# Performance work log

Measured on AMD Instinct MI355X. Metric: run time of the kernel, lower is better.

Reference implementation:

```python
import jax, jax.numpy as jnp
import numpy as np

T, B, F = 512, 256, 1
H = 256          # hidden width of all GRU stacks
P = 256          # pred_classes
DELAY = 1
W_SCALE = 0.06   # ~1/sqrt(H), mimics torch GRUCell init scale


def setup_inputs() -> dict:
    key = jax.random.key(0)
    ks = jax.random.split(key, 24)
    rn = lambda k, shp, s=1.0: s * jax.random.normal(k, shp, dtype=jnp.float32)
    return {
        "sequence": rn(ks[0], (T, B, F)),
        "delay_pad": rn(ks[1], (DELAY, B, F)),
        "h0_enc": rn(ks[2], (B, H)),
        "h0_mask": rn(ks[3], (B, H)),
        "h0_pred": rn(ks[4], (B, H)),
        "enc_w_ih": rn(ks[5], (3 * H, F), W_SCALE),
        "enc_w_hh": rn(ks[6], (3 * H, H), W_SCALE),
        "enc_b_ih": rn(ks[7], (3 * H,), W_SCALE),
        "enc_b_hh": rn(ks[8], (3 * H,), W_SCALE),
        "mdec_w_ih": rn(ks[9], (3 * H, H), W_SCALE),
        "mdec_w_hh": rn(ks[10], (3 * H, H), W_SCALE),
        "mdec_b_ih": rn(ks[11], (3 * H,), W_SCALE),
        "mdec_b_hh": rn(ks[12], (3 * H,), W_SCALE),
        "mlin_w": rn(ks[13], (F, H), W_SCALE),
        "mlin_b": rn(ks[14], (F,), W_SCALE),
        "pdec_w_ih": rn(ks[15], (3 * H, H), W_SCALE),
        "pdec_w_hh": rn(ks[16], (3 * H, H), W_SCALE),
        "pdec_b_ih": rn(ks[17], (3 * H,), W_SCALE),
        "pdec_b_hh": rn(ks[18], (3 * H,), W_SCALE),
        "plin_w": rn(ks[19], (P, H), W_SCALE),
        "plin_b": rn(ks[20], (P,), W_SCALE),
    }


def gru_cell(x, h, w_ih, w_hh, b_ih, b_hh):
    # torch.nn.GRUCell semantics; gate order r, z, n in the stacked weights.
    gi = x @ w_ih.T + b_ih           # [B, 3H]
    gh = h @ w_hh.T + b_hh           # [B, 3H]
    i_r, i_z, i_n = jnp.split(gi, 3, axis=-1)
    h_r, h_z, h_n = jnp.split(gh, 3, axis=-1)
    r = jax.nn.sigmoid(i_r + h_r)
    z = jax.nn.sigmoid(i_z + h_z)
    n = jnp.tanh(i_n + r * h_n)
    return (1.0 - z) * n + z * h


def reference(sequence, delay_pad, h0_enc, h0_mask, h0_pred,
              enc_w_ih, enc_w_hh, enc_b_ih, enc_b_hh,
              mdec_w_ih, mdec_w_hh, mdec_b_ih, mdec_b_hh, mlin_w, mlin_b,
              pdec_w_ih, pdec_w_hh, pdec_b_ih, pdec_b_hh, plin_w, plin_b):
    # delay: prepend padding, drop last `delay` steps.  seq stays [T, B, F].
    seq = jnp.concatenate([delay_pad, sequence[:-DELAY]], axis=0)

    def step(carry, x_t):
        h_e, h_m, h_p = carry
        h_e = gru_cell(x_t, h_e, enc_w_ih, enc_w_hh, enc_b_ih, enc_b_hh)
        h_m = gru_cell(h_e, h_m, mdec_w_ih, mdec_w_hh, mdec_b_ih, mdec_b_hh)
        mask_t = h_m @ mlin_w.T + mlin_b      # [B, F]
        h_p = gru_cell(h_e, h_p, pdec_w_ih, pdec_w_hh, pdec_b_ih, pdec_b_hh)
        pred_t = h_p @ plin_w.T + plin_b      # [B, P]
        return (h_e, h_m, h_p), (mask_t, pred_t)

    _, (masks, preds) = jax.lax.scan(step, (h0_enc, h0_mask, h0_pred), seq)
    mask = masks.reshape(seq.shape)           # [T, B, F]
    pred = jnp.mean(preds, axis=0)            # [B, P]
    return mask, pred
```

## Files before the change

kernel.cpp:

```cpp
#include <hip/hip_runtime.h>
#include <hip/hip_fp16.h>

typedef _Float16 f16;
typedef _Float16 f16x8 __attribute__((ext_vector_type(8)));
typedef _Float16 f16x4 __attribute__((ext_vector_type(4)));
typedef float    f32x4 __attribute__((ext_vector_type(4)));

#define TT 512
#define BB 256
#define HH 256

#define O_WFRAG_ENC 0u
#define O_WFRAG_M   393216u
#define O_WFRAG_P   786432u
#define O_WFRAG_GI  1179648u
#define O_HE_ST     1966080u
#define O_HM_ST     2097152u
#define O_HP_ST     2228224u
#define O_HPSUM     2359296u
#define O_DYN       2621440u
#define DYN_PER_STEP 917504u

__device__ __forceinline__ float sigf(float x){ return 1.0f/(1.0f+__expf(-x)); }
__device__ __forceinline__ float tanh_(float x){
  float xc = fminf(fmaxf(x,-15.f),15.f);
  float e  = __expf(2.f*xc);
  return (e-1.f)/(e+1.f);
}
__device__ __forceinline__ int hswz(int row, int j){
  return row*256 + ((((j>>3) ^ (row&7)))<<3) + (j&7);
}
__device__ __forceinline__ void gload_lds16(const void* g, void* l){
  __builtin_amdgcn_global_load_lds(
      (const __attribute__((address_space(1))) unsigned int*)g,
      (__attribute__((address_space(3))) unsigned int*)l, 16, 0, 0);
}
#define SB()        __builtin_amdgcn_sched_barrier(0)
#define LGKM0_SB()  do{ asm volatile("s_waitcnt lgkmcnt(0)" ::: "memory"); SB(); }while(0)
#define WAITV6_SB() do{ asm volatile("s_waitcnt vmcnt(6)"   ::: "memory"); SB(); }while(0)

__global__ void prep_kernel(
    const float* __restrict__ enc_whh, const float* __restrict__ mdec_whh,
    const float* __restrict__ pdec_whh, const float* __restrict__ mdec_wih,
    const float* __restrict__ pdec_wih,
    const float* __restrict__ h0e, const float* __restrict__ h0m, const float* __restrict__ h0p,
    f16* __restrict__ wfrag_enc, f16* __restrict__ wfrag_m, f16* __restrict__ wfrag_p,
    f16* __restrict__ wfrag_gi,
    f16* __restrict__ he_st, f16* __restrict__ hm_st, f16* __restrict__ hp_st,
    float* __restrict__ hpsum)
{
  int idx = blockIdx.x*256 + threadIdx.x;
  const int NW = 8*48*64*8;
  if (idx < 3*NW){
    int b = idx / NW, e = idx % NW;
    int jj = e & 7, l = (e>>3)&63, c = e>>9;
    int ks = c / 48, rem = c % 48;
    int w = rem / 3, g = rem % 3;
    int row = g*256 + w*16 + (l&15);
    int col = ks*32 + (l>>4)*8 + jj;
    const float* W = (b==0)?enc_whh:((b==1)?mdec_whh:pdec_whh);
    f16* D = (b==0)?wfrag_enc:((b==1)?wfrag_m:wfrag_p);
    D[e] = (f16)W[row*256+col];
    return;
  }
  idx -= 3*NW;
  const int NG = 96*8*64*8;
  if (idx < NG){
    int e = idx;
    int jj = e&7, l=(e>>3)&63, ks=(e>>9)&7, mt = e>>12;
    int row = mt*16 + (l&15);
    int col = ks*32 + (l>>4)*8 + jj;
    float v = (row < 768) ? mdec_wih[row*256+col] : pdec_wih[(row-768)*256+col];
    wfrag_gi[e] = (f16)v;
    return;
  }
  idx -= NG;
  if (idx < 65536){
    he_st[idx] = (f16)h0e[idx];
    hm_st[idx] = (f16)h0m[idx];
    hp_st[idx] = (f16)h0p[idx];
    hpsum[idx] = 0.f;
  }
}

template<int MODE>
__device__ __forceinline__ void gru_run(
  int bt, int slice, int SL,
  const f16* __restrict__ wfrag,
  const float* __restrict__ bih, const float* __restrict__ bhh,
  const float* __restrict__ enc_wih,
  const float* __restrict__ seq, const float* __restrict__ dpad,
  const f16* __restrict__ gi_src,
  f16* __restrict__ h_state,
  f16* __restrict__ he_buf,
  const float* __restrict__ mlin_w, const float* __restrict__ mlin_b,
  float* __restrict__ out_mask,
  float* __restrict__ hpsum,
  unsigned char* smem)
{
  const int tid = threadIdx.x;
  const int lane = tid & 63;
  const int wid  = tid >> 6;
  const int l15  = lane & 15;
  const int lhi  = lane >> 4;
  const int bi0  = lhi*4;
  const int b0   = bt*16;
  const int w0   = wid*2;

  f16* wbuf = (f16*)smem;
  f16* hbuf = (f16*)(smem + 98304);
  float* xb   = (float*)(smem + 98304 + 16384);
  float* mred = xb + 32;

  float cr[2], cz[2], cnh[2], cni[2];
  float wr_[2], wz_[2], wn_[2], mw[2];
  #pragma unroll
  for (int q=0;q<2;++q){
    const int j = (w0+q)*16 + l15;
    if (MODE==0){
      cr[q]  = bih[j]     + bhh[j];
      cz[q]  = bih[256+j] + bhh[256+j];
      cnh[q] = bhh[512+j];
      cni[q] = bih[512+j];
      wr_[q]=enc_wih[j]; wz_[q]=enc_wih[256+j]; wn_[q]=enc_wih[512+j];
    } else {
      cr[q]  = bhh[j];
      cz[q]  = bhh[256+j];
      cnh[q] = bhh[512+j];
      cni[q] = 0.f;
    }
    if (MODE==1){ mw[q]=mlin_w[j]; }
  }
  #pragma unroll
  for (int q=0;q<2;++q){
    const int j = (w0+q)*16 + l15;
    #pragma unroll
    for (int r=0;r<4;++r)
      hbuf[hswz(bi0+r, j)] = h_state[(size_t)(b0+bi0+r)*256 + j];
  }
  if (MODE==0 && tid<16){
    const int t = slice*SL;
    xb[tid] = (t==0) ? dpad[b0+tid] : seq[(size_t)(t-1)*BB + b0 + tid];
  }
  #pragma unroll
  for (int q=0;q<2;++q)
    #pragma unroll
    for (int g=0;g<3;++g){
      const int fo = ((w0+q)*3+g)*1024;
      gload_lds16((const char*)wfrag + fo + (lane<<4), (char*)wbuf + fo);
    }
  __syncthreads();

  float psum[2][4];
  if (MODE==2){
    #pragma unroll
    for (int q=0;q<2;++q)
      #pragma unroll
      for (int r=0;r<4;++r) psum[q][r]=0.f;
  }

  for (int ts=0; ts<SL; ++ts){
    const int cur = ts & 1;
    f16* hc = hbuf + cur*4096;
    f16* hn = hbuf + (cur^1)*4096;

    f16x4 gv[2][3];
    if (MODE!=0){
      const f16* gts = gi_src + (size_t)ts*393216u;
      #pragma unroll
      for (int q=0;q<2;++q)
        #pragma unroll
        for (int g=0;g<3;++g)
          gv[q][g] = *(const f16x4*)(gts + ((size_t)(g*256 + (w0+q)*16 + l15))*16 + bi0);
    } else if (tid<16 && ts+1<SL){
      xb[(cur^1)*16 + tid] = seq[(size_t)(slice*SL + ts)*BB + b0 + tid];
    }
    if (MODE==1 && tid<16 && ts>0){
      float v = mlin_b[0];
      #pragma unroll
      for (int w=0;w<8;++w) v += mred[(cur^1)*128 + w*16 + tid];
      out_mask[(size_t)(slice*SL + ts-1)*BB + b0 + tid] = v;
    }

    f32x4 acc[2][3];
    #pragma unroll
    for (int q=0;q<2;++q){
      acc[q][0] = (f32x4){cr[q],cr[q],cr[q],cr[q]};
      acc[q][1] = (f32x4){cz[q],cz[q],cz[q],cz[q]};
      acc[q][2] = (f32x4){cnh[q],cnh[q],cnh[q],cnh[q]};
    }
    #pragma unroll
    for (int k=0;k<8;++k){
      LGKM0_SB();
      {
        const int nk = (k<7) ? (k+1) : 0;
        const char* src = (const char*)wfrag + (size_t)nk*49152u;
        char* dst = (char*)wbuf + (nk&1)*49152;
        #pragma unroll
        for (int q=0;q<2;++q)
          #pragma unroll
          for (int g=0;g<3;++g){
            const int fo = ((w0+q)*3+g)*1024;
            gload_lds16(src + fo + (lane<<4), dst + fo);
          }
      }
      SB();
      if (k>0) WAITV6_SB();

      const f16* wb = wbuf + (k&1)*24576;
      const f16x8 a = *(const f16x8*)(hc + l15*256 + ((((k*4+lhi) ^ (l15&7)))<<3));
      #pragma unroll
      for (int q=0;q<2;++q)
        #pragma unroll
        for (int g=0;g<3;++g){
          const f16x8 b = *(const f16x8*)(wb + (((w0+q)*3+g)*64 + lane)*8);
          acc[q][g] = __builtin_amdgcn_mfma_f32_16x16x32_f16(a, b, acc[q][g], 0,0,0);
        }
    }

    float mpart[4] = {0.f,0.f,0.f,0.f};
    #pragma unroll
    for (int q=0;q<2;++q){
      const int j = (w0+q)*16 + l15;
      float gir[4], giz[4], gin[4];
      if (MODE==0){
        #pragma unroll
        for (int r=0;r<4;++r){
          const float x = xb[cur*16 + bi0 + r];
          gir[r]=x*wr_[q]; giz[r]=x*wz_[q]; gin[r]=x*wn_[q] + cni[q];
        }
      } else {
        #pragma unroll
        for (int r=0;r<4;++r){
          gir[r]=(float)gv[q][0][r]; giz[r]=(float)gv[q][1][r]; gin[r]=(float)gv[q][2][r];
        }
      }
      #pragma unroll
      for (int r=0;r<4;++r){
        const int sz = hswz(bi0+r, j);
        const float hprev = (float)hc[sz];
        const float rr = sigf(gir[r] + acc[q][0][r]);
        const float zz = sigf(giz[r] + acc[q][1][r]);
        const float nn = tanh_(gin[r] + rr*acc[q][2][r]);
        const float h  = (1.f-zz)*nn + zz*hprev;
        hn[sz] = (f16)h;
        if (MODE==0) he_buf[((size_t)ts*BB + (b0+bi0+r))*HH + j] = (f16)h;
        if (MODE==1) mpart[r] += h*mw[q];
        if (MODE==2) psum[q][r] += h;
      }
    }
    if (MODE==1){
      #pragma unroll
      for (int m=1;m<16;m<<=1){
        #pragma unroll
        for (int r=0;r<4;++r) mpart[r] += __shfl_xor(mpart[r], m, 64);
      }
      if (l15==0){
        #pragma unroll
        for (int r=0;r<4;++r) mred[cur*128 + wid*16 + bi0 + r] = mpart[r];
      }
    }
    __syncthreads();
  }

  if (MODE==1 && tid<16){
    float v = mlin_b[0];
    #pragma unroll
    for (int w=0;w<8;++w) v += mred[((SL-1)&1)*128 + w*16 + tid];
    out_mask[(size_t)(slice*SL + SL-1)*BB + b0 + tid] = v;
  }
  {
    const f16* hf = hbuf + (SL&1)*4096;
    #pragma unroll
    for (int q=0;q<2;++q){
      const int j = (w0+q)*16 + l15;
      #pragma unroll
      for (int r=0;r<4;++r)
        h_state[(size_t)(b0+bi0+r)*256 + j] = hf[hswz(bi0+r, j)];
    }
  }
  if (MODE==2){
    #pragma unroll
    for (int q=0;q<2;++q){
      const int j = (w0+q)*16 + l15;
      #pragma unroll
      for (int r=0;r<4;++r){
        const size_t idx = (size_t)(b0+bi0+r)*256 + j;
        hpsum[idx] = hpsum[idx] + psum[q][r];
      }
    }
  }
}

__global__ __launch_bounds__(512) void rec_kernel(
  const float* __restrict__ seq, const float* __restrict__ dpad,
  const float* __restrict__ enc_wih, const float* __restrict__ enc_bih, const float* __restrict__ enc_bhh,
  const float* __restrict__ mdec_bhh, const float* __restrict__ pdec_bhh,
  const float* __restrict__ mlin_w, const float* __restrict__ mlin_b,
  const f16* __restrict__ wfrag_enc, const f16* __restrict__ wfrag_m, const f16* __restrict__ wfrag_p,
  f16* __restrict__ he_st, f16* __restrict__ hm_st, f16* __restrict__ hp_st,
  f16* __restrict__ he_buf, const f16* __restrict__ gi_buf,
  float* __restrict__ hpsum, float* __restrict__ out_mask,
  int dec_slice, int enc_slice, int SL)
{
  __shared__ __align__(16) unsigned char smem[98304 + 16384 + 128 + 1024 + 256];
  const int pp = blockIdx.x;
  if (pp < 16){
    if (dec_slice < 0) return;
    const int bt = pp;
    gru_run<1>(bt, dec_slice, SL, wfrag_m, nullptr, mdec_bhh, nullptr, nullptr, nullptr,
               gi_buf + (size_t)bt*1536*16, hm_st, nullptr, mlin_w, mlin_b, out_mask, nullptr, smem);
  } else if (pp < 32){
    if (dec_slice < 0) return;
    const int bt = pp - 16;
    gru_run<2>(bt, dec_slice, SL, wfrag_p, nullptr, pdec_bhh, nullptr, nullptr, nullptr,
               gi_buf + ((size_t)bt*1536 + 768)*16, hp_st, nullptr, nullptr, nullptr, nullptr, hpsum, smem);
  } else {
    if (enc_slice < 0) return;
    const int bt = pp - 32;
    gru_run<0>(bt, enc_slice, SL, wfrag_enc, enc_bih, enc_bhh, enc_wih, seq, dpad,
               nullptr, he_st, he_buf, nullptr, nullptr, nullptr, nullptr, smem);
  }
}

__global__ __launch_bounds__(256,4) void gi_kernel(
  const f16* __restrict__ he_buf, const f16* __restrict__ wfrag_gi,
  const float* __restrict__ mdec_bih, const float* __restrict__ pdec_bih,
  f16* __restrict__ gi_buf)
{
  const int ts = blockIdx.x >> 2;
  const int bq = blockIdx.x & 3;
  const int tid = threadIdx.x, lane = tid&63, wid = tid>>6;
  const int l15 = lane&15, lhi = lane>>4;
  __shared__ f16 het[64*264];
  {
    const uint4* src = (const uint4*)(he_buf + ((size_t)ts*BB + bq*64)*HH);
    uint4* dst = (uint4*)het;
    #pragma unroll
    for (int k=0;k<8;++k){
      const int i = tid + k*256;
      dst[(i>>5)*33 + (i&31)] = src[i];
    }
  }
  __syncthreads();
  for (int mi=0; mi<24; ++mi){
    const int mt = wid*24 + mi;
    const int row0 = mt*16 + lhi*4;
    float bb[4];
    #pragma unroll
    for (int r=0;r<4;++r){
      const int rw = row0 + r;
      bb[r] = (rw < 768) ? mdec_bih[rw] : pdec_bih[rw-768];
    }
    f32x4 acc[4] = {{0,0,0,0},{0,0,0,0},{0,0,0,0},{0,0,0,0}};
    #pragma unroll
    for (int ks=0;ks<8;++ks){
      const f16x8 a = *(const f16x8*)(wfrag_gi + ((size_t)(mt*8+ks)*64 + lane)*8);
      #pragma unroll
      for (int bt=0;bt<4;++bt){
        const f16x8 b = *(const f16x8*)(het + (bt*16+l15)*264 + ks*32 + lhi*8);
        acc[bt] = __builtin_amdgcn_mfma_f32_16x16x32_f16(a, b, acc[bt], 0,0,0);
      }
    }
    #pragma unroll
    for (int bt=0;bt<4;++bt){
      const int btg = bq*4 + bt;
      const size_t base = (((size_t)ts*16 + btg)*1536 + (size_t)mt*16 + lhi*4)*16 + l15;
      #pragma unroll
      for (int r=0;r<4;++r) gi_buf[base + (size_t)r*16] = (f16)(acc[bt][r] + bb[r]);
    }
  }
}

__global__ __launch_bounds__(256,1) void pred_kernel(
  const float* __restrict__ hpsum, const float* __restrict__ plin_w,
  const float* __restrict__ plin_b, float* __restrict__ out)
{
  __shared__ float hs[256];
  const int p = threadIdx.x;
  const float bias = plin_b[p];
  for (int bb=0; bb<4; ++bb){
    const int b = blockIdx.x*4 + bb;
    __syncthreads();
    hs[p] = hpsum[(size_t)b*256 + p];
    __syncthreads();
    float acc = 0.f;
    const float4* wrow = (const float4*)(plin_w + (size_t)p*256);
    #pragma unroll 4
    for (int k4=0;k4<64;++k4){
      const float4 w = wrow[k4];
      acc += hs[k4*4+0]*w.x + hs[k4*4+1]*w.y + hs[k4*4+2]*w.z + hs[k4*4+3]*w.w;
    }
    out[131072 + (size_t)b*256 + p] = acc*(1.f/512.f) + bias;
  }
}

extern "C" void kernel_launch(void* const* d_in, const int* in_sizes, int n_in,
                              void* d_out, int out_size, void* d_ws, size_t ws_size,
                              hipStream_t stream)
{
  const float* seq      = (const float*)d_in[0];
  const float* dpad     = (const float*)d_in[1];
  const float* h0e      = (const float*)d_in[2];
  const float* h0m      = (const float*)d_in[3];
  const float* h0p      = (const float*)d_in[4];
  const float* enc_wih  = (const float*)d_in[5];
  const float* enc_whh  = (const float*)d_in[6];
  const float* enc_bih  = (const float*)d_in[7];
  const float* enc_bhh  = (const float*)d_in[8];
  const float* mdec_wih = (const float*)d_in[9];
  const float* mdec_whh = (const float*)d_in[10];
  const float* mdec_bih = (const float*)d_in[11];
  const float* mdec_bhh = (const float*)d_in[12];
  const float* mlin_w   = (const float*)d_in[13];
  const float* mlin_b   = (const float*)d_in[14];
  const float* pdec_wih = (const float*)d_in[15];
  const float* pdec_whh = (const float*)d_in[16];
  const float* pdec_bih = (const float*)d_in[17];
  const float* pdec_bhh = (const float*)d_in[18];
  const float* plin_w   = (const float*)d_in[19];
  const float* plin_b   = (const float*)d_in[20];
  float* out = (float*)d_out;

  char* ws = (char*)d_ws;
  f16* wfrag_enc = (f16*)(ws + O_WFRAG_ENC);
  f16* wfrag_m   = (f16*)(ws + O_WFRAG_M);
  f16* wfrag_p   = (f16*)(ws + O_WFRAG_P);
  f16* wfrag_gi  = (f16*)(ws + O_WFRAG_GI);
  f16* he_st     = (f16*)(ws + O_HE_ST);
  f16* hm_st     = (f16*)(ws + O_HM_ST);
  f16* hp_st     = (f16*)(ws + O_HP_ST);
  float* hpsum   = (float*)(ws + O_HPSUM);

  int SL = 64;
  while (SL > 1 && (size_t)O_DYN + (size_t)SL*DYN_PER_STEP > ws_size) SL >>= 1;
  const int S = TT / SL;
  f16* he_buf = (f16*)(ws + O_DYN);
  f16* gi_buf = (f16*)(ws + O_DYN + (size_t)SL*131072u);

  prep_kernel<<<dim3(4096), dim3(256), 0, stream>>>(
      enc_whh, mdec_whh, pdec_whh, mdec_wih, pdec_wih, h0e, h0m, h0p,
      wfrag_enc, wfrag_m, wfrag_p, wfrag_gi, he_st, hm_st, hp_st, hpsum);

  rec_kernel<<<dim3(48), dim3(512), 0, stream>>>(
      seq, dpad, enc_wih, enc_bih, enc_bhh, mdec_bhh, pdec_bhh,
      mlin_w, mlin_b, wfrag_enc, wfrag_m, wfrag_p, he_st, hm_st, hp_st,
      he_buf, gi_buf, hpsum, out, -1, 0, SL);
  gi_kernel<<<dim3(SL*4), dim3(256), 0, stream>>>(he_buf, wfrag_gi, mdec_bih, pdec_bih, gi_buf);

  for (int s=0; s<S; ++s){
    const int enc_s = (s+1 < S) ? (s+1) : -1;
    rec_kernel<<<dim3(48), dim3(512), 0, stream>>>(
        seq, dpad, enc_wih, enc_bih, enc_bhh, mdec_bhh, pdec_bhh,
        mlin_w, mlin_b, wfrag_enc, wfrag_m, wfrag_p, he_st, hm_st, hp_st,
        he_buf, gi_buf, hpsum, out, s, enc_s, SL);
    if (enc_s >= 0)
      gi_kernel<<<dim3(SL*4), dim3(256), 0, stream>>>(he_buf, wfrag_gi, mdec_bih, pdec_bih, gi_buf);
  }

  pred_kernel<<<dim3(64), dim3(256), 0, stream>>>(hpsum, plin_w, plin_b, out);
}
```

Before: 3.615 ms.

## Process 32 batch rows per recurrent block to halve weight streaming

```diff
diff --git a/kernel.cpp b/kernel.cpp
--- a/kernel.cpp
+++ b/kernel.cpp
@@ -85,12 +85,12 @@
 
 template<int MODE>
 __device__ __forceinline__ void gru_run(
-  int bt, int slice, int SL,
+  int g32, int slice, int SL,
   const f16* __restrict__ wfrag,
   const float* __restrict__ bih, const float* __restrict__ bhh,
   const float* __restrict__ enc_wih,
   const float* __restrict__ seq, const float* __restrict__ dpad,
-  const f16* __restrict__ gi_src,
+  const f16* __restrict__ gi_buf,
   f16* __restrict__ h_state,
   f16* __restrict__ he_buf,
   const float* __restrict__ mlin_w, const float* __restrict__ mlin_b,
@@ -104,13 +104,15 @@
   const int l15  = lane & 15;
   const int lhi  = lane >> 4;
   const int bi0  = lhi*4;
-  const int b0   = bt*16;
+  const int b0   = g32*32;
   const int w0   = wid*2;
-
-  f16* wbuf = (f16*)smem;
-  f16* hbuf = (f16*)(smem + 98304);
-  float* xb   = (float*)(smem + 98304 + 16384);
-  float* mred = xb + 32;
+  const int GOFF = (MODE==2) ? 768 : 0;
+
+  f16* wbuf  = (f16*)smem;
+  f16* hbuf  = (f16*)(smem + 98304);
+  float* ps  = (float*)(smem + 114688);
+  float* mred= (float*)(smem + 147456);
+  float* xb  = (float*)(smem + 148480);
 
   float cr[2], cz[2], cnh[2], cni[2];
   float wr_[2], wz_[2], wn_[2], mw[2];
@@ -131,14 +133,21 @@
     }
     if (MODE==1){ mw[q]=mlin_w[j]; }
   }
+  const float mlb = (MODE==1) ? mlin_b[0] : 0.f;
+
   #pragma unroll
   for (int q=0;q<2;++q){
     const int j = (w0+q)*16 + l15;
     #pragma unroll
-    for (int r=0;r<4;++r)
-      hbuf[hswz(bi0+r, j)] = h_state[(size_t)(b0+bi0+r)*256 + j];
-  }
-  if (MODE==0 && tid<16){
+    for (int rt=0;rt<2;++rt)
+      #pragma unroll
+      for (int r=0;r<4;++r){
+        const int row = rt*16 + bi0 + r;
+        hbuf[hswz(row, j)] = h_state[(size_t)(b0+row)*256 + j];
+        if (MODE==2) ps[row*256 + j] = 0.f;
+      }
+  }
+  if (MODE==0 && tid<32){
     const int t = slice*SL;
     xb[tid] = (t==0) ? dpad[b0+tid] : seq[(size_t)(t-1)*BB + b0 + tid];
   }
@@ -151,44 +160,35 @@
     }
   __syncthreads();
 
-  float psum[2][4];
-  if (MODE==2){
-    #pragma unroll
-    for (int q=0;q<2;++q)
-      #pragma unroll
-      for (int r=0;r<4;++r) psum[q][r]=0.f;
-  }
-
   for (int ts=0; ts<SL; ++ts){
     const int cur = ts & 1;
-    f16* hc = hbuf + cur*4096;
-    f16* hn = hbuf + (cur^1)*4096;
-
-    f16x4 gv[2][3];
+
+    f16x4 gv[2][3][2];
     if (MODE!=0){
-      const f16* gts = gi_src + (size_t)ts*393216u;
-      #pragma unroll
-      for (int q=0;q<2;++q)
-        #pragma unroll
-        for (int g=0;g<3;++g)
-          gv[q][g] = *(const f16x4*)(gts + ((size_t)(g*256 + (w0+q)*16 + l15))*16 + bi0);
-    } else if (tid<16 && ts+1<SL){
-      xb[(cur^1)*16 + tid] = seq[(size_t)(slice*SL + ts)*BB + b0 + tid];
-    }
-    if (MODE==1 && tid<16 && ts>0){
-      float v = mlin_b[0];
-      #pragma unroll
-      for (int w=0;w<8;++w) v += mred[(cur^1)*128 + w*16 + tid];
-      out_mask[(size_t)(slice*SL + ts-1)*BB + b0 + tid] = v;
-    }
-
-    f32x4 acc[2][3];
-    #pragma unroll
-    for (int q=0;q<2;++q){
-      acc[q][0] = (f32x4){cr[q],cr[q],cr[q],cr[q]};
-      acc[q][1] = (f32x4){cz[q],cz[q],cz[q],cz[q]};
-      acc[q][2] = (f32x4){cnh[q],cnh[q],cnh[q],cnh[q]};
-    }
+      #pragma unroll
+      for (int rt=0;rt<2;++rt){
+        const size_t tb = ((size_t)ts*16 + (g32*2+rt))*24576u;
+        #pragma unroll
+        for (int q=0;q<2;++q)
+          #pragma unroll
+          for (int g=0;g<3;++g){
+            const size_t n = (size_t)(GOFF + g*256 + (w0+q)*16 + l15);
+            gv[q][g][rt] = *(const f16x4*)(gi_buf + tb + n*16 + bi0);
+          }
+      }
+    } else if (tid<32 && ts+1<SL){
+      xb[(cur^1)*32 + tid] = seq[(size_t)(slice*SL + ts)*BB + b0 + tid];
+    }
+
+    f32x4 acc[2][3][2];
+    #pragma unroll
+    for (int q=0;q<2;++q)
+      #pragma unroll
+      for (int rt=0;rt<2;++rt){
+        acc[q][0][rt] = (f32x4){cr[q],cr[q],cr[q],cr[q]};
+        acc[q][1][rt] = (f32x4){cz[q],cz[q],cz[q],cz[q]};
+        acc[q][2][rt] = (f32x4){cnh[q],cnh[q],cnh[q],cnh[q]};
+      }
     #pragma unroll
     for (int k=0;k<8;++k){
       LGKM0_SB();
@@ -208,87 +208,87 @@
       if (k>0) WAITV6_SB();
 
       const f16* wb = wbuf + (k&1)*24576;
-      const f16x8 a = *(const f16x8*)(hc + l15*256 + ((((k*4+lhi) ^ (l15&7)))<<3));
+      const int koff = (((k*4+lhi) ^ (l15&7))<<3);
+      const f16x8 a0 = *(const f16x8*)(hbuf + (     l15)*256 + koff);
+      const f16x8 a1 = *(const f16x8*)(hbuf + (16 + l15)*256 + koff);
       #pragma unroll
       for (int q=0;q<2;++q)
         #pragma unroll
         for (int g=0;g<3;++g){
           const f16x8 b = *(const f16x8*)(wb + (((w0+q)*3+g)*64 + lane)*8);
-          acc[q][g] = __builtin_amdgcn_mfma_f32_16x16x32_f16(a, b, acc[q][g], 0,0,0);
+          acc[q][g][0] = __builtin_amdgcn_mfma_f32_16x16x32_f16(a0, b, acc[q][g][0], 0,0,0);
+          acc[q][g][1] = __builtin_amdgcn_mfma_f32_16x16x32_f16(a1, b, acc[q][g][1], 0,0,0);
         }
     }
-
-    float mpart[4] = {0.f,0.f,0.f,0.f};
+    __syncthreads();
+
+    float mpart[2][4] = {{0,0,0,0},{0,0,0,0}};
     #pragma unroll
     for (int q=0;q<2;++q){
       const int j = (w0+q)*16 + l15;
-      float gir[4], giz[4], gin[4];
-      if (MODE==0){
+      #pragma unroll
+      for (int rt=0;rt<2;++rt)
         #pragma unroll
         for (int r=0;r<4;++r){
-          const float x = xb[cur*16 + bi0 + r];
-          gir[r]=x*wr_[q]; giz[r]=x*wz_[q]; gin[r]=x*wn_[q] + cni[q];
+          const int row = rt*16 + bi0 + r;
+          const int sz = hswz(row, j);
+          const float hprev = (float)hbuf[sz];
+          float gir, giz, gin;
+          if (MODE==0){
+            const float x = xb[cur*32 + row];
+            gir = x*wr_[q]; giz = x*wz_[q]; gin = x*wn_[q] + cni[q];
+          } else {
+            gir = (float)gv[q][0][rt][r];
+            giz = (float)gv[q][1][rt][r];
+            gin = (float)gv[q][2][rt][r];
+          }
+          const float rr = sigf(gir + acc[q][0][rt][r]);
+          const float zz = sigf(giz + acc[q][1][rt][r]);
+          const float nn = tanh_(gin + rr*acc[q][2][rt][r]);
+          const float h  = (1.f-zz)*nn + zz*hprev;
+          hbuf[sz] = (f16)h;
+          if (MODE==0) he_buf[((size_t)ts*BB + (b0+row))*HH + j] = (f16)h;
+          if (MODE==1) mpart[rt][r] += h*mw[q];
+          if (MODE==2) ps[row*256 + j] += h;
         }
-      } else {
-        #pragma unroll
-        for (int r=0;r<4;++r){
-          gir[r]=(float)gv[q][0][r]; giz[r]=(float)gv[q][1][r]; gin[r]=(float)gv[q][2][r];
+    }
+    if (MODE==1){
+      #pragma unroll
+      for (int m=1;m<16;m<<=1)
+        #pragma unroll
+        for (int rt=0;rt<2;++rt)
+          #pragma unroll
+          for (int r=0;r<4;++r) mpart[rt][r] += __shfl_xor(mpart[rt][r], m, 64);
+      if (l15==0){
+        #pragma unroll
+        for (int rt=0;rt<2;++rt)
+          #pragma unroll
+          for (int r=0;r<4;++r) mred[wid*32 + rt*16 + bi0 + r] = mpart[rt][r];
+      }
+    }
+    __syncthreads();
+    if (MODE==1 && tid<32){
+      float v = mlb;
+      #pragma unroll
+      for (int w=0;w<8;++w) v += mred[w*32 + tid];
+      out_mask[(size_t)(slice*SL + ts)*BB + b0 + tid] = v;
+    }
+  }
+
+  #pragma unroll
+  for (int q=0;q<2;++q){
+    const int j = (w0+q)*16 + l15;
+    #pragma unroll
+    for (int rt=0;rt<2;++rt)
+      #pragma unroll
+      for (int r=0;r<4;++r){
+        const int row = rt*16 + bi0 + r;
+        h_state[(size_t)(b0+row)*256 + j] = hbuf[hswz(row, j)];
+        if (MODE==2){
+          const size_t idx = (size_t)(b0+row)*256 + j;
+          hpsum[idx] = hpsum[idx] + ps[row*256 + j];
         }
       }
-      #pragma unroll
-      for (int r=0;r<4;++r){
-        const int sz = hswz(bi0+r, j);
-        const float hprev = (float)hc[sz];
-        const float rr = sigf(gir[r] + acc[q][0][r]);
-        const float zz = sigf(giz[r] + acc[q][1][r]);
-        const float nn = tanh_(gin[r] + rr*acc[q][2][r]);
-        const float h  = (1.f-zz)*nn + zz*hprev;
-        hn[sz] = (f16)h;
-        if (MODE==0) he_buf[((size_t)ts*BB + (b0+bi0+r))*HH + j] = (f16)h;
-        if (MODE==1) mpart[r] += h*mw[q];
-        if (MODE==2) psum[q][r] += h;
-      }
-    }
-    if (MODE==1){
-      #pragma unroll
-      for (int m=1;m<16;m<<=1){
-        #pragma unroll
-        for (int r=0;r<4;++r) mpart[r] += __shfl_xor(mpart[r], m, 64);
-      }
-      if (l15==0){
-        #pragma unroll
-        for (int r=0;r<4;++r) mred[cur*128 + wid*16 + bi0 + r] = mpart[r];
-      }
-    }
-    __syncthreads();
-  }
-
-  if (MODE==1 && tid<16){
-    float v = mlin_b[0];
-    #pragma unroll
-    for (int w=0;w<8;++w) v += mred[((SL-1)&1)*128 + w*16 + tid];
-    out_mask[(size_t)(slice*SL + SL-1)*BB + b0 + tid] = v;
-  }
-  {
-    const f16* hf = hbuf + (SL&1)*4096;
-    #pragma unroll
-    for (int q=0;q<2;++q){
-      const int j = (w0+q)*16 + l15;
-      #pragma unroll
-      for (int r=0;r<4;++r)
-        h_state[(size_t)(b0+bi0+r)*256 + j] = hf[hswz(bi0+r, j)];
-    }
-  }
-  if (MODE==2){
-    #pragma unroll
-    for (int q=0;q<2;++q){
-      const int j = (w0+q)*16 + l15;
-      #pragma unroll
-      for (int r=0;r<4;++r){
-        const size_t idx = (size_t)(b0+bi0+r)*256 + j;
-        hpsum[idx] = hpsum[idx] + psum[q][r];
-      }
-    }
   }
 }
 
@@ -303,22 +303,19 @@
   float* __restrict__ hpsum, float* __restrict__ out_mask,
   int dec_slice, int enc_slice, int SL)
 {
-  __shared__ __align__(16) unsigned char smem[98304 + 16384 + 128 + 1024 + 256];
-  const int pp = blockIdx.x;
-  if (pp < 16){
+  __shared__ __align__(16) unsigned char smem[148736];
+  const int rec = blockIdx.x >> 3, g32 = blockIdx.x & 7;
+  if (rec == 0){
     if (dec_slice < 0) return;
-    const int bt = pp;
-    gru_run<1>(bt, dec_slice, SL, wfrag_m, nullptr, mdec_bhh, nullptr, nullptr, nullptr,
-               gi_buf + (size_t)bt*1536*16, hm_st, nullptr, mlin_w, mlin_b, out_mask, nullptr, smem);
-  } else if (pp < 32){
+    gru_run<1>(g32, dec_slice, SL, wfrag_m, nullptr, mdec_bhh, nullptr, nullptr, nullptr,
+               gi_buf, hm_st, nullptr, mlin_w, mlin_b, out_mask, nullptr, smem);
+  } else if (rec == 1){
     if (dec_slice < 0) return;
-    const int bt = pp - 16;
-    gru_run<2>(bt, dec_slice, SL, wfrag_p, nullptr, pdec_bhh, nullptr, nullptr, nullptr,
-               gi_buf + ((size_t)bt*1536 + 768)*16, hp_st, nullptr, nullptr, nullptr, nullptr, hpsum, smem);
+    gru_run<2>(g32, dec_slice, SL, wfrag_p, nullptr, pdec_bhh, nullptr, nullptr, nullptr,
+               gi_buf, hp_st, nullptr, nullptr, nullptr, nullptr, hpsum, smem);
   } else {
     if (enc_slice < 0) return;
-    const int bt = pp - 32;
-    gru_run<0>(bt, enc_slice, SL, wfrag_enc, enc_bih, enc_bhh, enc_wih, seq, dpad,
+    gru_run<0>(g32, enc_slice, SL, wfrag_enc, enc_bih, enc_bhh, enc_wih, seq, dpad,
                nullptr, he_st, he_buf, nullptr, nullptr, nullptr, nullptr, smem);
   }
 }
@@ -442,7 +439,7 @@
       enc_whh, mdec_whh, pdec_whh, mdec_wih, pdec_wih, h0e, h0m, h0p,
       wfrag_enc, wfrag_m, wfrag_p, wfrag_gi, he_st, hm_st, hp_st, hpsum);
 
-  rec_kernel<<<dim3(48), dim3(512), 0, stream>>>(
+  rec_kernel<<<dim3(24), dim3(512), 0, stream>>>(
       seq, dpad, enc_wih, enc_bih, enc_bhh, mdec_bhh, pdec_bhh,
       mlin_w, mlin_b, wfrag_enc, wfrag_m, wfrag_p, he_st, hm_st, hp_st,
       he_buf, gi_buf, hpsum, out, -1, 0, SL);
@@ -450,7 +447,7 @@
 
   for (int s=0; s<S; ++s){
     const int enc_s = (s+1 < S) ? (s+1) : -1;
-    rec_kernel<<<dim3(48), dim3(512), 0, stream>>>(
+    rec_kernel<<<dim3(24), dim3(512), 0, stream>>>(
         seq, dpad, enc_wih, enc_bih, enc_bhh, mdec_bhh, pdec_bhh,
         mlin_w, mlin_b, wfrag_enc, wfrag_m, wfrag_p, he_st, hm_st, hp_st,
         he_buf, gi_buf, hpsum, out, s, enc_s, SL);
```

After: 6.217 ms. +72.0%, slower.
